# Performance work log

Hardware: AMD Instinct MI355X
Metric: run time of the kernel (lower is better)

## Reference

```python
import jax, jax.numpy as jnp
import numpy as np

DIM = 64
HEADS = 4
DIM_HEAD = 32
HIDDEN = HEADS * DIM_HEAD  # 128
EPS = 1e-5


def _layernorm_ch(x, g, b):
    # channel-dim LayerNorm (biased var), x: [b, c, n]
    mean = jnp.mean(x, axis=1, keepdims=True)
    var = jnp.var(x, axis=1, keepdims=True)  # unbiased=False
    return (x - mean) / jnp.sqrt(var + EPS) * g.reshape(1, -1, 1) + b.reshape(1, -1, 1)


def setup_inputs() -> dict:
    key = jax.random.key(0)
    ks = jax.random.split(key, 4)
    x = jax.random.normal(ks[0], (2, DIM, 32, 64, 64), dtype=jnp.float32)
    # 1x1x1 convs are channel matmuls; store weights as [out_ch, in_ch]
    w_qkv = jax.random.normal(ks[1], (HIDDEN * 3, DIM), dtype=jnp.float32) * (1.0 / np.sqrt(DIM))
    w_out = jax.random.normal(ks[2], (DIM, HIDDEN), dtype=jnp.float32) * (1.0 / np.sqrt(HIDDEN))
    b_out = jax.random.normal(ks[3], (DIM,), dtype=jnp.float32) * 0.02
    g1 = jnp.ones((DIM,), dtype=jnp.float32)
    b1 = jnp.zeros((DIM,), dtype=jnp.float32)
    g2 = jnp.ones((DIM,), dtype=jnp.float32)
    b2 = jnp.zeros((DIM,), dtype=jnp.float32)
    return {"x": x, "g1": g1, "b1": b1, "w_qkv": w_qkv, "w_out": w_out,
            "b_out": b_out, "g2": g2, "b2": b2}


def reference(x, g1, b1, w_qkv, w_out, b_out, g2, b2):
    b, c, *spatial = x.shape
    n = int(np.prod(spatial))
    scale = DIM_HEAD ** -0.5

    xf = x.reshape(b, c, n)
    xn = _layernorm_ch(xf, g1, b1)

    # 1x1x1 conv qkv projection (no bias)
    qkv = jnp.einsum('oc,bcn->bon', w_qkv, xn)  # [b, 3*hidden, n]
    qkv = qkv.reshape(b, 3, HEADS, DIM_HEAD, n)
    q, k, v = qkv[:, 0], qkv[:, 1], qkv[:, 2]   # each [b, h, d, n]

    q = jax.nn.softmax(q, axis=2) * scale       # softmax over dim_head
    k = jax.nn.softmax(k, axis=3)               # softmax over tokens

    ctx = jnp.einsum('bhdn,bhen->bhde', k, v)   # [b, h, d, e] small
    out = jnp.einsum('bhde,bhdn->bhen', ctx, q) # [b, h, e, n]
    out = out.reshape(b, HIDDEN, n)

    y = jnp.einsum('oc,bcn->bon', w_out, out) + b_out.reshape(1, -1, 1)
    y = _layernorm_ch(y, g2, b2)
    return y.reshape(b, c, *spatial)
```

## Files before the change

kernel.cpp:

```cpp
#include <hip/hip_runtime.h>

#define NCOL 131072
#define CH 64

typedef float floatx4 __attribute__((ext_vector_type(4)));
typedef __bf16 bf16x8 __attribute__((ext_vector_type(8)));
typedef unsigned int u32x4 __attribute__((ext_vector_type(4)));
typedef unsigned int u32x2 __attribute__((ext_vector_type(2)));

union FragU { u32x4 q; bf16x8 v; unsigned short us[8]; };

__device__ __forceinline__ unsigned short bfb(float f){
  union { __bf16 h; unsigned short s; } u; u.h = (__bf16)f; return u.s;
}
__device__ __forceinline__ float bf2f(unsigned short h){
  union { unsigned u; float f; } x{(unsigned)h << 16};
  return x.f;
}

__device__ __forceinline__ void ln_stage(const float* __restrict__ xp,
    const float* __restrict__ g, const float* __restrict__ bb,
    unsigned short* __restrict__ xn_s, int t)
{
  float xv[64]; float s = 0.f, ss = 0.f;
  #pragma unroll
  for (int c = 0; c < 64; c++){ float u = xp[(long)c*NCOL]; xv[c] = u; s += u; ss = fmaf(u,u,ss); }
  const float mean = s * (1.f/64.f);
  const float rstd = rsqrtf(ss * (1.f/64.f) - mean*mean + 1e-5f);
  #pragma unroll
  for (int c = 0; c < 64; c++) xv[c] = (xv[c]-mean)*rstd*g[c] + bb[c];
  #pragma unroll
  for (int j = 0; j < 8; j++){
    FragU u;
    #pragma unroll
    for (int e = 0; e < 8; e++) u.v[e] = (__bf16)xv[j*8+e];
    *(u32x4*)(xn_s + t*72 + j*8) = u.q;
  }
}

__global__ __launch_bounds__(256) void kW(
    const float* __restrict__ wqkv, unsigned short* __restrict__ wbf, float* __restrict__ Oz)
{
  const int i = blockIdx.x*256 + threadIdx.x;
  wbf[i] = bfb(wqkv[i]);
  if (i < 8448) Oz[i] = 0.f;
}

__global__ __launch_bounds__(256) void kA(
    const float* __restrict__ x, const float* __restrict__ g1, const float* __restrict__ b1,
    const unsigned short* __restrict__ wbf, float* __restrict__ pctx, float* __restrict__ Zg)
{
  __shared__ __align__(16) char smem[37888];
  unsigned short* xn_s = (unsigned short*)smem;
  unsigned short* ek_s = (unsigned short*)smem;
  unsigned short* v_s  = (unsigned short*)(smem + 16896);
  float* Zp            = (float*)(smem + 33792);

  const int t = threadIdx.x;
  const int bid = blockIdx.x;
  const int b = bid >> 9;
  const long col0 = (long)(bid & 511) * 256;
  const int w = t >> 6, lane = t & 63, qq = lane >> 4, l16 = lane & 15;

  ln_stage(x + (long)b*CH*NCOL + col0 + t, g1, b1, xn_s, t);
  __syncthreads();

  FragU bx[4][2];
  #pragma unroll
  for (int nt = 0; nt < 4; nt++)
    #pragma unroll
    for (int ks = 0; ks < 2; ks++)
      bx[nt][ks].q = *(const u32x4*)(xn_s + ((4*w+nt)*16 + l16)*72 + ks*32 + qq*8);
  __syncthreads();

  floatx4 cc[4][2][2];
  #pragma unroll
  for (int h = 0; h < 4; h++)
    #pragma unroll
    for (int dt = 0; dt < 2; dt++)
      #pragma unroll
      for (int et = 0; et < 2; et++)
        cc[h][dt][et] = floatx4{0.f,0.f,0.f,0.f};

  #pragma unroll
  for (int h = 0; h < 4; h++){
    #pragma unroll
    for (int rt = 0; rt < 4; rt++){
      const int row0 = ((rt < 2) ? 128 : 256) + h*32 + (rt & 1)*16;
      const unsigned short* wr = wbf + (row0 + l16)*64 + qq*8;
      FragU a0, a1;
      a0.q = *(const u32x4*)wr;
      a1.q = *(const u32x4*)(wr + 32);
      unsigned short* dst = ((rt < 2) ? ek_s : v_s) + ((rt & 1)*16 + qq*4)*264;
      #pragma unroll
      for (int nt = 0; nt < 4; nt++){
        floatx4 c = floatx4{0.f,0.f,0.f,0.f};
        c = __builtin_amdgcn_mfma_f32_16x16x32_bf16(a0.v, bx[nt][0].v, c, 0, 0, 0);
        c = __builtin_amdgcn_mfma_f32_16x16x32_bf16(a1.v, bx[nt][1].v, c, 0, 0, 0);
        const int colb = (4*w+nt)*16 + l16;
        if (rt < 2){
          #pragma unroll
          for (int r = 0; r < 4; r++) dst[r*264 + colb] = bfb(__expf(c[r]));
        } else {
          #pragma unroll
          for (int r = 0; r < 4; r++) dst[r*264 + colb] = bfb(c[r]);
        }
      }
    }
    __syncthreads();
    {
      const int d = t & 31, part = t >> 5;
      const unsigned short* p = ek_s + d*264 + part*32;
      float zs = 0.f;
      #pragma unroll
      for (int j = 0; j < 4; j++){
        FragU u; u.q = *(const u32x4*)(p + j*8);
        #pragma unroll
        for (int e = 0; e < 8; e++) zs += bf2f(u.us[e]);
      }
      Zp[h*256 + part*32 + d] = zs;
    }
    #pragma unroll
    for (int kk = 0; kk < 2; kk++){
      const int ks2 = 2*w + kk;
      FragU ae[2], bv[2];
      #pragma unroll
      for (int dt = 0; dt < 2; dt++) ae[dt].q = *(const u32x4*)(ek_s + (dt*16 + l16)*264 + ks2*32 + qq*8);
      #pragma unroll
      for (int et = 0; et < 2; et++) bv[et].q = *(const u32x4*)(v_s + (et*16 + l16)*264 + ks2*32 + qq*8);
      #pragma unroll
      for (int dt = 0; dt < 2; dt++)
        #pragma unroll
        for (int et = 0; et < 2; et++)
          cc[h][dt][et] = __builtin_amdgcn_mfma_f32_16x16x32_bf16(ae[dt].v, bv[et].v, cc[h][dt][et], 0, 0, 0);
    }
    __syncthreads();
  }

  float* scr = (float*)smem;
  if (w & 1){
    #pragma unroll
    for (int h = 0; h < 4; h++)
      #pragma unroll
      for (int dt = 0; dt < 2; dt++)
        #pragma unroll
        for (int et = 0; et < 2; et++)
          ((floatx4*)scr)[(w>>1)*1024 + (h*4 + dt*2 + et)*64 + lane] = cc[h][dt][et];
  }
  __syncthreads();
  if (!(w & 1)){
    #pragma unroll
    for (int h = 0; h < 4; h++)
      #pragma unroll
      for (int dt = 0; dt < 2; dt++)
        #pragma unroll
        for (int et = 0; et < 2; et++)
          cc[h][dt][et] += ((floatx4*)scr)[(w>>1)*1024 + (h*4 + dt*2 + et)*64 + lane];
  }
  __syncthreads();
  if (w == 2){
    #pragma unroll
    for (int h = 0; h < 4; h++)
      #pragma unroll
      for (int dt = 0; dt < 2; dt++)
        #pragma unroll
        for (int et = 0; et < 2; et++)
          ((floatx4*)scr)[(h*4 + dt*2 + et)*64 + lane] = cc[h][dt][et];
  }
  __syncthreads();
  if (w == 0){
    #pragma unroll
    for (int h = 0; h < 4; h++)
      #pragma unroll
      for (int dt = 0; dt < 2; dt++)
        #pragma unroll
        for (int et = 0; et < 2; et++){
          floatx4 r = cc[h][dt][et] + ((floatx4*)scr)[(h*4 + dt*2 + et)*64 + lane];
          *(floatx4*)(pctx + (long)bid*4096 + (h*4 + dt*2 + et)*256 + lane*4) = r;
        }
  }
  if (t < 128){
    const int h = t >> 5, d = t & 31;
    float z = 0.f;
    #pragma unroll
    for (int part = 0; part < 8; part++) z += Zp[h*256 + part*32 + d];
    atomicAdd(&Zg[b*128 + h*32 + d], z);
  }
}

__global__ __launch_bounds__(256) void kR1(
    const float* __restrict__ pctx, float* __restrict__ O)
{
  const int blk = blockIdx.x;
  const int b = blk >> 7;
  const int part = (blk >> 4) & 7;
  const int chunk = blk & 15;
  const int t = threadIdx.x;
  const int r = chunk*256 + t;
  const float* p = pctx + ((long)(b*512 + part*64))*4096 + r;
  float s = 0.f;
  #pragma unroll 16
  for (int row = 0; row < 64; row++) s += p[(long)row*4096];
  atomicAdd(&O[b*4096 + r], s);
}

__global__ __launch_bounds__(256) void kM(
    const float* __restrict__ O, const float* __restrict__ Zg,
    const float* __restrict__ wout, unsigned short* __restrict__ Mgbf)
{
  const int idx = blockIdx.x*256 + threadIdx.x;
  const int b = idx >> 13, rem = idx & 8191;
  const int h = rem >> 11, o = (rem >> 5) & 63, dd = rem & 31;
  const int dt = dd >> 4, qq = (dd >> 2) & 3, rg = dd & 3;
  float m = 0.f;
  #pragma unroll
  for (int ee = 0; ee < 32; ee++){
    const int et = ee >> 4, l16 = ee & 15;
    const int r = h*1024 + (dt*2 + et)*256 + (qq*16 + l16)*4 + rg;
    m = fmaf(wout[o*128 + h*32 + ee], O[b*4096 + r], m);
  }
  m /= Zg[b*128 + h*32 + dd];
  Mgbf[idx] = bfb(m);
}

__global__ __launch_bounds__(256) void kB(
    const float* __restrict__ x, const float* __restrict__ g1, const float* __restrict__ b1,
    const unsigned short* __restrict__ wbf, const unsigned short* __restrict__ Mgbf,
    const float* __restrict__ bout, const float* __restrict__ g2, const float* __restrict__ b2,
    float* __restrict__ y)
{
  __shared__ __align__(16) char smem[37632];
  unsigned short* xn_s = (unsigned short*)smem;
  unsigned short* qs_s = (unsigned short*)smem;
  float* sp            = (float*)(smem + 36864);

  const int t = threadIdx.x;
  const int bid = blockIdx.x;
  const int b = bid >> 9;
  const long col0 = (long)(bid & 511) * 256;
  const int w = t >> 6, lane = t & 63, qq = lane >> 4, l16 = lane & 15;

  if (t < 64){ sp[t] = bout[t]; sp[64+t] = g2[t]; sp[128+t] = b2[t]; }
  ln_stage(x + (long)b*CH*NCOL + col0 + t, g1, b1, xn_s, t);
  __syncthreads();

  FragU bx[4][2];
  #pragma unroll
  for (int nt = 0; nt < 4; nt++)
    #pragma unroll
    for (int ks = 0; ks < 2; ks++)
      bx[nt][ks].q = *(const u32x4*)(xn_s + ((4*w+nt)*16 + l16)*72 + ks*32 + qq*8);
  __syncthreads();

  floatx4 yacc[4][4];
  #pragma unroll
  for (int ot = 0; ot < 4; ot++)
    #pragma unroll
    for (int nt = 0; nt < 4; nt++)
      yacc[ot][nt] = floatx4{0.f,0.f,0.f,0.f};

  #pragma unroll
  for (int h = 0; h < 4; h++){
    #pragma unroll
    for (int ot = 0; ot < 2; ot++){
      const int row0 = h*32 + ot*16;
      const unsigned short* wr = wbf + (row0 + l16)*64 + qq*8;
      FragU a0, a1;
      a0.q = *(const u32x4*)wr;
      a1.q = *(const u32x4*)(wr + 32);
      #pragma unroll
      for (int nt = 0; nt < 4; nt++){
        floatx4 c = floatx4{0.f,0.f,0.f,0.f};
        c = __builtin_amdgcn_mfma_f32_16x16x32_bf16(a0.v, bx[nt][0].v, c, 0, 0, 0);
        c = __builtin_amdgcn_mfma_f32_16x16x32_bf16(a1.v, bx[nt][1].v, c, 0, 0, 0);
        const int colb = (4*w+nt)*16 + l16;
        const unsigned short p0 = bfb(__expf(c[0])), p1 = bfb(__expf(c[1]));
        const unsigned short p2 = bfb(__expf(c[2])), p3 = bfb(__expf(c[3]));
        u32x2 pk; pk[0] = (unsigned)p0 | ((unsigned)p1 << 16); pk[1] = (unsigned)p2 | ((unsigned)p3 << 16);
        *(u32x2*)(qs_s + colb*40 + ot*16 + qq*4) = pk;
      }
    }
    __syncthreads();
    {
      unsigned short* p = qs_s + t*40;
      FragU u[4]; float s = 0.f;
      #pragma unroll
      for (int j = 0; j < 4; j++){
        u[j].q = *(const u32x4*)(p + j*8);
        #pragma unroll
        for (int e = 0; e < 8; e++) s += bf2f(u[j].us[e]);
      }
      const float sc = 0.17677669529663687f / s;
      #pragma unroll
      for (int j = 0; j < 4; j++){
        #pragma unroll
        for (int e = 0; e < 8; e++) u[j].v[e] = (__bf16)(bf2f(u[j].us[e]) * sc);
        *(u32x4*)(p + j*8) = u[j].q;
      }
    }
    __syncthreads();
    #pragma unroll
    for (int ot = 0; ot < 4; ot++){
      FragU am;
      am.q = *(const u32x4*)(Mgbf + (((long)b*4 + h)*64 + ot*16 + l16)*32 + qq*8);
      #pragma unroll
      for (int nt = 0; nt < 4; nt++){
        FragU bq; bq.q = *(const u32x4*)(qs_s + ((4*w+nt)*16 + l16)*40 + qq*8);
        yacc[ot][nt] = __builtin_amdgcn_mfma_f32_16x16x32_bf16(am.v, bq.v, yacc[ot][nt], 0, 0, 0);
      }
    }
    __syncthreads();
  }

  const long ybase = (long)b*CH*NCOL;
  #pragma unroll
  for (int nt = 0; nt < 4; nt++){
    const long colg = col0 + (4*w+nt)*16 + l16;
    float vals[16]; float s = 0.f, ss = 0.f;
    #pragma unroll
    for (int ot = 0; ot < 4; ot++)
      #pragma unroll
      for (int r = 0; r < 4; r++){
        const float v = yacc[ot][nt][r] + sp[ot*16 + qq*4 + r];
        vals[ot*4+r] = v; s += v; ss = fmaf(v, v, ss);
      }
    s  += __shfl_xor(s, 16, 64);  s  += __shfl_xor(s, 32, 64);
    ss += __shfl_xor(ss, 16, 64); ss += __shfl_xor(ss, 32, 64);
    const float mean = s * (1.f/64.f);
    const float rstd = rsqrtf(ss * (1.f/64.f) - mean*mean + 1e-5f);
    #pragma unroll
    for (int ot = 0; ot < 4; ot++)
      #pragma unroll
      for (int r = 0; r < 4; r++){
        const int row = ot*16 + qq*4 + r;
        y[ybase + (long)row*NCOL + colg] = (vals[ot*4+r]-mean)*rstd*sp[64+row] + sp[128+row];
      }
  }
}

extern "C" void kernel_launch(void* const* d_in, const int* in_sizes, int n_in,
                              void* d_out, int out_size, void* d_ws, size_t ws_size,
                              hipStream_t stream)
{
  const float* x    = (const float*)d_in[0];
  const float* g1   = (const float*)d_in[1];
  const float* b1   = (const float*)d_in[2];
  const float* wqkv = (const float*)d_in[3];
  const float* wout = (const float*)d_in[4];
  const float* bout = (const float*)d_in[5];
  const float* g2   = (const float*)d_in[6];
  const float* b2   = (const float*)d_in[7];
  float* y  = (float*)d_out;
  float* ws = (float*)d_ws;

  float* pctx = ws;
  float* O    = ws + 4194304;
  float* Zg   = O + 8192;
  unsigned short* Mgbf = (unsigned short*)(Zg + 256);
  unsigned short* wbf  = (unsigned short*)(ws + 4210944);

  hipLaunchKernelGGL(kW,  dim3(96),   dim3(256), 0, stream, wqkv, wbf, O);
  hipLaunchKernelGGL(kA,  dim3(1024), dim3(256), 0, stream, x, g1, b1, wbf, pctx, Zg);
  hipLaunchKernelGGL(kR1, dim3(256),  dim3(256), 0, stream, pctx, O);
  hipLaunchKernelGGL(kM,  dim3(64),   dim3(256), 0, stream, O, Zg, wout, Mgbf);
  hipLaunchKernelGGL(kB,  dim3(1024), dim3(256), 0, stream, x, g1, b1, wbf, Mgbf, bout, g2, b2, y);
}
```

Measured before the change: 235.0 us.

## Make softmax sums wave-local and drop block barriers in attention kernels

In the context kernel, the exp(k) column sums are accumulated in registers during the projection and reduced with wave shuffles, replacing a pass that re-read LDS. Each wave only touches its own LDS columns, so the per-head __syncthreads are removed. In the output kernel, both 16-row halves of each q head are computed together, so the softmax over dim_head is normalized in registers with cross-lane shuffles before the LDS store. This removes the separate LDS normalization pass and its barriers. It relies on LDS data being wave-private and adds register pressure.

```diff
diff --git a/kernel.cpp b/kernel.cpp
--- a/kernel.cpp
+++ b/kernel.cpp
@@ -63,8 +63,6 @@
   const int w = t >> 6, lane = t & 63, qq = lane >> 4, l16 = lane & 15;
 
   ln_stage(x + (long)b*CH*NCOL + col0 + t, g1, b1, xn_s, t);
-  __syncthreads();
-
   FragU bx[4][2];
   #pragma unroll
   for (int nt = 0; nt < 4; nt++)
@@ -84,6 +82,9 @@
 
   #pragma unroll
   for (int h = 0; h < 4; h++){
+    float zr[8];
+    #pragma unroll
+    for (int j = 0; j < 8; j++) zr[j] = 0.f;
     #pragma unroll
     for (int rt = 0; rt < 4; rt++){
       const int row0 = ((rt < 2) ? 128 : 256) + h*32 + (rt & 1)*16;
@@ -100,25 +101,23 @@
         const int colb = (4*w+nt)*16 + l16;
         if (rt < 2){
           #pragma unroll
-          for (int r = 0; r < 4; r++) dst[r*264 + colb] = bfb(__expf(c[r]));
+          for (int r = 0; r < 4; r++){
+            const float e = __expf(c[r]);
+            dst[r*264 + colb] = bfb(e);
+            zr[(rt & 1)*4 + r] += e;
+          }
         } else {
           #pragma unroll
           for (int r = 0; r < 4; r++) dst[r*264 + colb] = bfb(c[r]);
         }
       }
     }
-    __syncthreads();
-    {
-      const int d = t & 31, part = t >> 5;
-      const unsigned short* p = ek_s + d*264 + part*32;
-      float zs = 0.f;
-      #pragma unroll
-      for (int j = 0; j < 4; j++){
-        FragU u; u.q = *(const u32x4*)(p + j*8);
-        #pragma unroll
-        for (int e = 0; e < 8; e++) zs += bf2f(u.us[e]);
-      }
-      Zp[h*256 + part*32 + d] = zs;
+    #pragma unroll
+    for (int j = 0; j < 8; j++){
+      float v = zr[j];
+      v += __shfl_xor(v, 1, 64); v += __shfl_xor(v, 2, 64);
+      v += __shfl_xor(v, 4, 64); v += __shfl_xor(v, 8, 64);
+      if (l16 == 0) Zp[w*128 + h*32 + (j >> 2)*16 + qq*4 + (j & 3)] = v;
     }
     #pragma unroll
     for (int kk = 0; kk < 2; kk++){
@@ -134,7 +133,12 @@
         for (int et = 0; et < 2; et++)
           cc[h][dt][et] = __builtin_amdgcn_mfma_f32_16x16x32_bf16(ae[dt].v, bv[et].v, cc[h][dt][et], 0, 0, 0);
     }
-    __syncthreads();
+  }
+  __syncthreads();
+
+  if (t < 128){
+    const float z = Zp[t] + Zp[128 + t] + Zp[256 + t] + Zp[384 + t];
+    atomicAdd(&Zg[b*128 + t], z);
   }
 
   float* scr = (float*)smem;
@@ -178,13 +182,6 @@
           floatx4 r = cc[h][dt][et] + ((floatx4*)scr)[(h*4 + dt*2 + et)*64 + lane];
           *(floatx4*)(pctx + (long)bid*4096 + (h*4 + dt*2 + et)*256 + lane*4) = r;
         }
-  }
-  if (t < 128){
-    const int h = t >> 5, d = t & 31;
-    float z = 0.f;
-    #pragma unroll
-    for (int part = 0; part < 8; part++) z += Zp[h*256 + part*32 + d];
-    atomicAdd(&Zg[b*128 + h*32 + d], z);
   }
 }
 
@@ -242,8 +239,6 @@
 
   if (t < 64){ sp[t] = bout[t]; sp[64+t] = g2[t]; sp[128+t] = b2[t]; }
   ln_stage(x + (long)b*CH*NCOL + col0 + t, g1, b1, xn_s, t);
-  __syncthreads();
-
   FragU bx[4][2];
   #pragma unroll
   for (int nt = 0; nt < 4; nt++)
@@ -261,44 +256,37 @@
 
   #pragma unroll
   for (int h = 0; h < 4; h++){
-    #pragma unroll
-    for (int ot = 0; ot < 2; ot++){
-      const int row0 = h*32 + ot*16;
-      const unsigned short* wr = wbf + (row0 + l16)*64 + qq*8;
-      FragU a0, a1;
-      a0.q = *(const u32x4*)wr;
-      a1.q = *(const u32x4*)(wr + 32);
-      #pragma unroll
-      for (int nt = 0; nt < 4; nt++){
-        floatx4 c = floatx4{0.f,0.f,0.f,0.f};
-        c = __builtin_amdgcn_mfma_f32_16x16x32_bf16(a0.v, bx[nt][0].v, c, 0, 0, 0);
-        c = __builtin_amdgcn_mfma_f32_16x16x32_bf16(a1.v, bx[nt][1].v, c, 0, 0, 0);
-        const int colb = (4*w+nt)*16 + l16;
-        const unsigned short p0 = bfb(__expf(c[0])), p1 = bfb(__expf(c[1]));
-        const unsigned short p2 = bfb(__expf(c[2])), p3 = bfb(__expf(c[3]));
-        u32x2 pk; pk[0] = (unsigned)p0 | ((unsigned)p1 << 16); pk[1] = (unsigned)p2 | ((unsigned)p3 << 16);
-        *(u32x2*)(qs_s + colb*40 + ot*16 + qq*4) = pk;
-      }
-    }
-    __syncthreads();
+    FragU a00, a01, a10, a11;
     {
-      unsigned short* p = qs_s + t*40;
-      FragU u[4]; float s = 0.f;
-      #pragma unroll
-      for (int j = 0; j < 4; j++){
-        u[j].q = *(const u32x4*)(p + j*8);
-        #pragma unroll
-        for (int e = 0; e < 8; e++) s += bf2f(u[j].us[e]);
-      }
+      const unsigned short* wr0 = wbf + (h*32 + l16)*64 + qq*8;
+      const unsigned short* wr1 = wbf + (h*32 + 16 + l16)*64 + qq*8;
+      a00.q = *(const u32x4*)wr0; a01.q = *(const u32x4*)(wr0 + 32);
+      a10.q = *(const u32x4*)wr1; a11.q = *(const u32x4*)(wr1 + 32);
+    }
+    #pragma unroll
+    for (int nt = 0; nt < 4; nt++){
+      floatx4 c0 = floatx4{0.f,0.f,0.f,0.f};
+      floatx4 c1 = floatx4{0.f,0.f,0.f,0.f};
+      c0 = __builtin_amdgcn_mfma_f32_16x16x32_bf16(a00.v, bx[nt][0].v, c0, 0, 0, 0);
+      c0 = __builtin_amdgcn_mfma_f32_16x16x32_bf16(a01.v, bx[nt][1].v, c0, 0, 0, 0);
+      c1 = __builtin_amdgcn_mfma_f32_16x16x32_bf16(a10.v, bx[nt][0].v, c1, 0, 0, 0);
+      c1 = __builtin_amdgcn_mfma_f32_16x16x32_bf16(a11.v, bx[nt][1].v, c1, 0, 0, 0);
+      float e[8]; float s = 0.f;
+      #pragma unroll
+      for (int r = 0; r < 4; r++){ e[r] = __expf(c0[r]); s += e[r]; }
+      #pragma unroll
+      for (int r = 0; r < 4; r++){ e[4+r] = __expf(c1[r]); s += e[4+r]; }
+      s += __shfl_xor(s, 16, 64); s += __shfl_xor(s, 32, 64);
       const float sc = 0.17677669529663687f / s;
-      #pragma unroll
-      for (int j = 0; j < 4; j++){
-        #pragma unroll
-        for (int e = 0; e < 8; e++) u[j].v[e] = (__bf16)(bf2f(u[j].us[e]) * sc);
-        *(u32x4*)(p + j*8) = u[j].q;
-      }
-    }
-    __syncthreads();
+      const int colb = (4*w+nt)*16 + l16;
+      u32x2 pk0, pk1;
+      pk0[0] = (unsigned)bfb(e[0]*sc) | ((unsigned)bfb(e[1]*sc) << 16);
+      pk0[1] = (unsigned)bfb(e[2]*sc) | ((unsigned)bfb(e[3]*sc) << 16);
+      pk1[0] = (unsigned)bfb(e[4]*sc) | ((unsigned)bfb(e[5]*sc) << 16);
+      pk1[1] = (unsigned)bfb(e[6]*sc) | ((unsigned)bfb(e[7]*sc) << 16);
+      *(u32x2*)(qs_s + colb*40 + qq*4)      = pk0;
+      *(u32x2*)(qs_s + colb*40 + 16 + qq*4) = pk1;
+    }
     #pragma unroll
     for (int ot = 0; ot < 4; ot++){
       FragU am;
@@ -309,7 +297,6 @@
         yacc[ot][nt] = __builtin_amdgcn_mfma_f32_16x16x32_bf16(am.v, bq.v, yacc[ot][nt], 0, 0, 0);
       }
     }
-    __syncthreads();
   }
 
   const long ybase = (long)b*CH*NCOL;
```

New measurement: 229.7 us. 1.02x faster.
